# Optimization experiments

Measured on AMD Instinct MI355X. Metric: run time of the kernel, lower is better.

## Reference

```python
import jax, jax.numpy as jnp
import numpy as np

B, T = 4, 1024
L, D_IN = 3, 1024          # num HM-LSTM layers, per-layer hidden size
D = L * D_IN               # concatenated hidden size (3072)
EMB = 2048                 # shared embedding size
N_LIN = 2                  # linear_sizes = [2048, 2048]
OUT = 32000                # vocab
SCALE = 0.02


def setup_inputs() -> dict:
    key = jax.random.key(0)
    ks = jax.random.split(key, 8)
    return {
        "x": jax.random.normal(ks[0], (B, T, D), jnp.float32),
        "w": jax.random.normal(ks[1], (L, D), jnp.float32) * SCALE,        # gate weights, one [D] vector per layer
        "emb_w": jax.random.normal(ks[2], (L, D_IN, EMB), jnp.float32) * SCALE,
        "emb_b": jax.random.normal(ks[3], (L, EMB), jnp.float32) * SCALE,
        "lin_w": jax.random.normal(ks[4], (N_LIN, EMB, EMB), jnp.float32) * SCALE,
        "lin_b": jax.random.normal(ks[5], (N_LIN, EMB), jnp.float32) * SCALE,
        "out_w": jax.random.normal(ks[6], (EMB, OUT), jnp.float32) * SCALE,
        "out_b": jax.random.normal(ks[7], (OUT,), jnp.float32) * SCALE,
    }


def reference(x, w, emb_w, emb_b, lin_w, lin_b, out_w, out_b):
    Bx, Tx, Dx = x.shape
    # Per-layer scalar gates: sg_l = h @ w_l, g = sigmoid(sg)  -> [B, T, L]
    g = jax.nn.sigmoid(jnp.einsum('btd,ld->btl', x, w))
    # Split concatenated hidden into layers: [B, T, L, D_IN]
    xl = x.reshape(Bx, Tx, L, D_IN)
    # s = sum_l Linear_l(h_l * g_l); biases sum across layers
    s = jnp.einsum('btl,btli,lie->bte', g, xl, emb_w) + emb_b.sum(axis=0)
    h = jax.nn.relu(s)
    # fnn: stacked linears with tanh activation after each
    for i in range(lin_w.shape[0]):
        h = jnp.tanh(h @ lin_w[i] + lin_b[i])
    # final output projection
    return h @ out_w + out_b
```

## Files before the change

kernel.cpp:

```cpp
#include <hip/hip_runtime.h>
#include <math.h>

typedef __attribute__((ext_vector_type(8))) short short8;
typedef __attribute__((ext_vector_type(8))) unsigned short ushort8;
typedef __attribute__((ext_vector_type(4))) unsigned short ushort4v;
typedef __attribute__((ext_vector_type(4))) unsigned int uint4v;
typedef __attribute__((ext_vector_type(4))) float f32x4;
typedef __attribute__((ext_vector_type(16))) float f32x16;

__device__ __forceinline__ unsigned short f2bf(float f) {
  union { float f; unsigned u; } v; v.f = f;
  unsigned u = v.u;
  return (unsigned short)((u + 0x7fffu + ((u >> 16) & 1u)) >> 16);
}

__device__ __forceinline__ void gload_lds16(const void* g, void* lds) {
  __builtin_amdgcn_global_load_lds(
      (const __attribute__((address_space(1))) unsigned int*)g,
      (__attribute__((address_space(3))) unsigned int*)lds, 16, 0, 0);
}

__device__ __forceinline__ void tc_body(const float* __restrict__ in,
                                        unsigned short* __restrict__ outp,
                                        int R, int C, int r0, int c0,
                                        char* smem) {
  float (*tile)[65] = (float(*)[65])smem;
  const int t = threadIdx.x;
  const int tr = t >> 4;
  const int tc = (t & 15) * 4;
#pragma unroll
  for (int p = 0; p < 4; ++p) {
    int r = p * 16 + tr;
    f32x4 v = *(const f32x4*)(in + (size_t)(r0 + r) * C + c0 + tc);
    tile[r][tc] = v[0]; tile[r][tc + 1] = v[1];
    tile[r][tc + 2] = v[2]; tile[r][tc + 3] = v[3];
  }
  __syncthreads();
  const int c = t >> 2;
  const int rb = (t & 3) * 16;
  ushort8 o0, o1;
#pragma unroll
  for (int j = 0; j < 8; ++j) o0[j] = f2bf(tile[rb + j][c]);
#pragma unroll
  for (int j = 0; j < 8; ++j) o1[j] = f2bf(tile[rb + 8 + j][c]);
  unsigned short* dst = outp + (size_t)(c0 + c) * R + r0 + rb;
  *(ushort8*)dst = o0;
  *(ushort8*)(dst + 8) = o1;
}

__global__ __launch_bounds__(256)
void gates_or_tc(const float* __restrict__ x, const float* __restrict__ w,
                 unsigned short* __restrict__ xg,
                 const float* __restrict__ emb_w, unsigned short* __restrict__ emb_wT,
                 const float* __restrict__ lin_w,
                 unsigned short* __restrict__ lin_wT0,
                 unsigned short* __restrict__ lin_wT1) {
  __shared__ __align__(16) char smem[64 * 65 * 4];
  __shared__ float sred[4][3];
  const int bid = blockIdx.x;
  const int t = threadIdx.x;

  if (bid >= 4096) {
    int b2 = bid - 4096;
    if (b2 < 1536) {
      tc_body(emb_w, emb_wT, 3072, 2048, (b2 >> 5) * 64, (b2 & 31) * 64, smem);
    } else {
      int b3 = b2 - 1536;
      const float* in = (b3 < 1024) ? lin_w : (lin_w + 2048 * 2048);
      unsigned short* outp = (b3 < 1024) ? lin_wT0 : lin_wT1;
      b3 &= 1023;
      tc_body(in, outp, 2048, 2048, (b3 >> 5) * 64, (b3 & 31) * 64, smem);
    }
    return;
  }

  const int n = bid;
  const float* xr = x + (size_t)n * 3072;
  f32x4 xv[3];
#pragma unroll
  for (int c = 0; c < 3; ++c)
    xv[c] = *(const f32x4*)(xr + c * 1024 + t * 4);

  float p[3] = {0.f, 0.f, 0.f};
#pragma unroll
  for (int l = 0; l < 3; ++l) {
#pragma unroll
    for (int c = 0; c < 3; ++c) {
      f32x4 wv = *(const f32x4*)(w + l * 3072 + c * 1024 + t * 4);
      p[l] += xv[c][0] * wv[0] + xv[c][1] * wv[1] + xv[c][2] * wv[2] + xv[c][3] * wv[3];
    }
  }
#pragma unroll
  for (int off = 32; off; off >>= 1) {
    p[0] += __shfl_xor(p[0], off);
    p[1] += __shfl_xor(p[1], off);
    p[2] += __shfl_xor(p[2], off);
  }
  const int wave = t >> 6, lane = t & 63;
  if (lane == 0) {
    sred[wave][0] = p[0]; sred[wave][1] = p[1]; sred[wave][2] = p[2];
  }
  __syncthreads();
  float g[3];
#pragma unroll
  for (int l = 0; l < 3; ++l) {
    float s = sred[0][l] + sred[1][l] + sred[2][l] + sred[3][l];
    g[l] = 1.f / (1.f + expf(-s));
  }
  unsigned short* orow = xg + (size_t)n * 3072;
#pragma unroll
  for (int c = 0; c < 3; ++c) {
    ushort4v o;
#pragma unroll
    for (int j = 0; j < 4; ++j) o[j] = f2bf(xv[c][j] * g[c]);
    *(ushort4v*)(orow + c * 1024 + t * 4) = o;
  }
}

__global__ __launch_bounds__(256)
void gemm0_or_tc(const unsigned short* __restrict__ A,
                 const unsigned short* __restrict__ Bt,
                 const float* __restrict__ bias,
                 unsigned short* __restrict__ Cb,
                 const float* __restrict__ tc_in,
                 unsigned short* __restrict__ tc_out,
                 int do_tc) {
  __shared__ __align__(16) char smem[32768];
  const int bid = blockIdx.x;

  if (bid >= 512) {
    int b2 = bid - 512;
    tc_body(tc_in, tc_out, 2048, 32000, (b2 / 500) * 64, (b2 % 500) * 64, smem);
    return;
  }
  (void)do_tc;

  unsigned short* As = (unsigned short*)smem;
  unsigned short* Bs = (unsigned short*)(smem + 16384);
  constexpr int K = 3072, N = 2048;

  const int tid = threadIdx.x;
  const int lane = tid & 63;
  const int wv = tid >> 6;
  const int wm = wv >> 1, wn = wv & 1;
  const int lid = (bid & 7) * 64 + (bid >> 3);
  const int mt = lid & 31;
  const int nt = lid >> 5;
  const int m0 = mt * 128, n0 = nt * 128;
  const size_t strideB = (size_t)K * 2;

  f32x4 acc[4][4] = {};

  for (int kt = 0; kt < K; kt += 64) {
    __syncthreads();
#pragma unroll
    for (int i = 0; i < 4; ++i) {
      const int o = wv * 4096 + i * 1024 + lane * 16;
      const int row = o >> 7;
      const int sw = (((o >> 4) & 7) * 16) ^ ((row & 7) << 4);
      gload_lds16((const char*)A + (size_t)(m0 + row) * strideB + (size_t)kt * 2 + sw,
                  (char*)As + wv * 4096 + i * 1024);
      gload_lds16((const char*)Bt + (size_t)(n0 + row) * strideB + (size_t)kt * 2 + sw,
                  (char*)Bs + wv * 4096 + i * 1024);
    }
    __syncthreads();
#pragma unroll
    for (int kk = 0; kk < 2; ++kk) {
      short8 av[4], bv[4];
      const int kb = kk * 64 + (lane >> 4) * 16;
#pragma unroll
      for (int mi = 0; mi < 4; ++mi) {
        int row = wm * 64 + mi * 16 + (lane & 15);
        av[mi] = *(const short8*)((const char*)As + row * 128 + (kb ^ ((row & 7) << 4)));
      }
#pragma unroll
      for (int ni = 0; ni < 4; ++ni) {
        int row = wn * 64 + ni * 16 + (lane & 15);
        bv[ni] = *(const short8*)((const char*)Bs + row * 128 + (kb ^ ((row & 7) << 4)));
      }
#pragma unroll
      for (int mi = 0; mi < 4; ++mi)
#pragma unroll
        for (int ni = 0; ni < 4; ++ni)
          acc[mi][ni] = __builtin_amdgcn_mfma_f32_16x16x32_bf16(av[mi], bv[ni], acc[mi][ni], 0, 0, 0);
    }
  }

  const int lr = lane >> 4, lc = lane & 15;
#pragma unroll
  for (int ni = 0; ni < 4; ++ni) {
    int c = n0 + wn * 64 + ni * 16 + lc;
    float bb = bias[c] + bias[N + c] + bias[2 * N + c];
#pragma unroll
    for (int mi = 0; mi < 4; ++mi) {
      int r0 = m0 + wm * 64 + mi * 16 + lr * 4;
      f32x4 v = acc[mi][ni];
#pragma unroll
      for (int j = 0; j < 4; ++j) {
        float val = v[j] + bb;
        val = val > 0.f ? val : 0.f;
        Cb[(size_t)(r0 + j) * N + c] = f2bf(val);
      }
    }
  }
}

template <int EPI>
__global__ __launch_bounds__(256)
void gemm_tt(const unsigned short* __restrict__ A,
             const unsigned short* __restrict__ Bt,
             const float* __restrict__ bias,
             unsigned short* __restrict__ Cb,
             float* __restrict__ Cf,
             int K, int N) {
  __shared__ __align__(16) unsigned short As[128 * 64];
  __shared__ __align__(16) unsigned short Bs[128 * 64];

  const int tid = threadIdx.x;
  const int lane = tid & 63;
  const int wv = tid >> 6;
  const int wm = wv >> 1, wn = wv & 1;
  const int bid = blockIdx.x;
  const int cpx = gridDim.x >> 3;
  const int lid = (bid & 7) * cpx + (bid >> 3);
  const int mt = lid & 31;
  const int nt = lid >> 5;
  const int m0 = mt * 128, n0 = nt * 128;
  const size_t strideB = (size_t)K * 2;

  f32x4 acc[4][4] = {};

  for (int kt = 0; kt < K; kt += 64) {
    __syncthreads();
#pragma unroll
    for (int i = 0; i < 4; ++i) {
      const int o = wv * 4096 + i * 1024 + lane * 16;
      const int row = o >> 7;
      const int sw = (((o >> 4) & 7) * 16) ^ ((row & 7) << 4);
      gload_lds16((const char*)A + (size_t)(m0 + row) * strideB + (size_t)kt * 2 + sw,
                  (char*)As + wv * 4096 + i * 1024);
      gload_lds16((const char*)Bt + (size_t)(n0 + row) * strideB + (size_t)kt * 2 + sw,
                  (char*)Bs + wv * 4096 + i * 1024);
    }
    __syncthreads();
#pragma unroll
    for (int kk = 0; kk < 2; ++kk) {
      short8 av[4], bv[4];
      const int kb = kk * 64 + (lane >> 4) * 16;
#pragma unroll
      for (int mi = 0; mi < 4; ++mi) {
        int row = wm * 64 + mi * 16 + (lane & 15);
        av[mi] = *(const short8*)((const char*)As + row * 128 + (kb ^ ((row & 7) << 4)));
      }
#pragma unroll
      for (int ni = 0; ni < 4; ++ni) {
        int row = wn * 64 + ni * 16 + (lane & 15);
        bv[ni] = *(const short8*)((const char*)Bs + row * 128 + (kb ^ ((row & 7) << 4)));
      }
#pragma unroll
      for (int mi = 0; mi < 4; ++mi)
#pragma unroll
        for (int ni = 0; ni < 4; ++ni)
          acc[mi][ni] = __builtin_amdgcn_mfma_f32_16x16x32_bf16(av[mi], bv[ni], acc[mi][ni], 0, 0, 0);
    }
  }

  const int lr = lane >> 4, lc = lane & 15;
#pragma unroll
  for (int ni = 0; ni < 4; ++ni) {
    int c = n0 + wn * 64 + ni * 16 + lc;
    float bb;
    if (EPI == 0) bb = bias[c] + bias[N + c] + bias[2 * N + c];
    else          bb = bias[c];
#pragma unroll
    for (int mi = 0; mi < 4; ++mi) {
      int r0 = m0 + wm * 64 + mi * 16 + lr * 4;
      f32x4 v = acc[mi][ni];
#pragma unroll
      for (int j = 0; j < 4; ++j) {
        float val = v[j] + bb;
        size_t idx = (size_t)(r0 + j) * N + c;
        if (EPI == 0) { val = val > 0.f ? val : 0.f; Cb[idx] = f2bf(val); }
        else if (EPI == 1) { Cb[idx] = f2bf(tanhf(val)); }
        else { Cf[idx] = val; }
      }
    }
  }
}

__global__ __launch_bounds__(512, 2)
void gemm8_out(const unsigned short* __restrict__ A,
               const unsigned short* __restrict__ Bt,
               const float* __restrict__ bias,
               float* __restrict__ Cf,
               int K, int N) {
  __shared__ __align__(16) unsigned short As8[2][256 * 64];
  __shared__ __align__(16) unsigned short Bs8[2][256 * 64];

  const int tid = threadIdx.x;
  const int lane = tid & 63;
  const int wid = tid >> 6;
  const int wm = wid >> 2, wn = wid & 3;

  const int bid = blockIdx.x;
  const int cpx = gridDim.x >> 3;
  const int lid = (bid & 7) * cpx + (bid >> 3);
  const int mt = lid & 15;
  const int ntile = lid >> 4;
  const int m0 = mt * 256, n0 = ntile * 256;
  const size_t strideB = (size_t)K * 2;
  const int kTiles = K >> 6;

  const unsigned short* smat = (wid < 4) ? A : Bt;
  char* sb = (wid < 4) ? (char*)As8 : (char*)Bs8;
  const int part = wid & 3;
  const int srow0 = ((wid < 4) ? m0 : n0) + part * 64 + (lane >> 3);
  const int ssw = ((lane & 7) ^ (lane >> 3)) << 4;

  auto stage8 = [&](int buf, int t) {
#pragma unroll
    for (int i = 0; i < 8; ++i)
      gload_lds16((const char*)smat + (size_t)(srow0 + i * 8) * strideB +
                      (size_t)t * 128 + ssw,
                  sb + buf * 32768 + part * 8192 + i * 1024);
  };

  const int l31 = lane & 31;
  const int hk16 = (lane >> 5) * 16;

  f32x16 acc[4][2] = {};

  stage8(0, 0);
  stage8(1, 1);
  asm volatile("s_waitcnt vmcnt(8)" ::: "memory");
  __builtin_amdgcn_sched_barrier(0);
  __builtin_amdgcn_s_barrier();

  for (int t = 0; t < kTiles; ++t) {
    const char* ab = (const char*)As8 + (t & 1) * 32768;
    const char* bb = (const char*)Bs8 + (t & 1) * 32768;
    short8 av[2][4], bva[4], bvb[4];

#pragma unroll
    for (int mi = 0; mi < 2; ++mi) {
      int r = wm * 128 + mi * 32 + l31;
      int sz = (r & 7) << 4;
#pragma unroll
      for (int ks = 0; ks < 4; ++ks)
        av[mi][ks] = *(const short8*)(ab + r * 128 + ((ks * 32 + hk16) ^ sz));
    }
    {
      int r = wn * 64 + l31;
      int sz = (r & 7) << 4;
#pragma unroll
      for (int ks = 0; ks < 4; ++ks)
        bva[ks] = *(const short8*)(bb + r * 128 + ((ks * 32 + hk16) ^ sz));
    }
    __builtin_amdgcn_s_setprio(1);
#pragma unroll
    for (int ks = 0; ks < 4; ++ks)
#pragma unroll
      for (int mi = 0; mi < 2; ++mi)
        acc[mi][0] = __builtin_amdgcn_mfma_f32_32x32x16_bf16(
            av[mi][ks], bva[ks], acc[mi][0], 0, 0, 0);
    __builtin_amdgcn_s_setprio(0);

    {
      int r = wn * 64 + 32 + l31;
      int sz = (r & 7) << 4;
#pragma unroll
      for (int ks = 0; ks < 4; ++ks)
        bvb[ks] = *(const short8*)(bb + r * 128 + ((ks * 32 + hk16) ^ sz));
    }
    __builtin_amdgcn_s_setprio(1);
#pragma unroll
    for (int ks = 0; ks < 4; ++ks)
#pragma unroll
      for (int mi = 0; mi < 2; ++mi)
        acc[mi][1] = __builtin_amdgcn_mfma_f32_32x32x16_bf16(
            av[mi][ks], bvb[ks], acc[mi][1], 0, 0, 0);
    __builtin_amdgcn_s_setprio(0);

#pragma unroll
    for (int mi = 0; mi < 2; ++mi) {
      int r = wm * 128 + 64 + mi * 32 + l31;
      int sz = (r & 7) << 4;
#pragma unroll
      for (int ks = 0; ks < 4; ++ks)
        av[mi][ks] = *(const short8*)(ab + r * 128 + ((ks * 32 + hk16) ^ sz));
    }
    __builtin_amdgcn_s_setprio(1);
#pragma unroll
    for (int ks = 0; ks < 4; ++ks)
#pragma unroll
      for (int mi = 0; mi < 2; ++mi)
        acc[2 + mi][1] = __builtin_amdgcn_mfma_f32_32x32x16_bf16(
            av[mi][ks], bvb[ks], acc[2 + mi][1], 0, 0, 0);
    __builtin_amdgcn_s_setprio(0);

    __builtin_amdgcn_s_setprio(1);
#pragma unroll
    for (int ks = 0; ks < 4; ++ks)
#pragma unroll
      for (int mi = 0; mi < 2; ++mi)
        acc[2 + mi][0] = __builtin_amdgcn_mfma_f32_32x32x16_bf16(
            av[mi][ks], bva[ks], acc[2 + mi][0], 0, 0, 0);
    __builtin_amdgcn_s_setprio(0);

    if (t + 1 < kTiles) {
      __builtin_amdgcn_sched_barrier(0);
      __builtin_amdgcn_s_barrier();
      if (t + 2 < kTiles) {
        stage8(t & 1, t + 2);
        asm volatile("s_waitcnt vmcnt(8)" ::: "memory");
      } else {
        asm volatile("s_waitcnt vmcnt(0)" ::: "memory");
      }
      __builtin_amdgcn_sched_barrier(0);
      __builtin_amdgcn_s_barrier();
    }
  }

  const int rbase = m0 + wm * 128 + 4 * (lane >> 5);
#pragma unroll
  for (int ni = 0; ni < 2; ++ni) {
    int c = n0 + wn * 64 + ni * 32 + l31;
    float bb2 = bias[c];
#pragma unroll
    for (int mi = 0; mi < 4; ++mi) {
#pragma unroll
      for (int rg = 0; rg < 16; ++rg) {
        int r = rbase + mi * 32 + (rg & 3) + 8 * (rg >> 2);
        __builtin_nontemporal_store(acc[mi][ni][rg] + bb2,
                                    &Cf[(size_t)r * N + c]);
      }
    }
  }
}

template <int EPI>
__global__ __launch_bounds__(256)
void gemm_bf16(const unsigned short* __restrict__ A,
               const float* __restrict__ B,
               const float* __restrict__ bias,
               unsigned short* __restrict__ Cb,
               float* __restrict__ Cf,
               int K, int N) {
  __shared__ __align__(16) unsigned short As[128 * 64];
  __shared__ __align__(16) unsigned short Bs[128 * 64];

  const int tid = threadIdx.x;
  const int lane = tid & 63;
  const int wv = tid >> 6;
  const int wm = wv >> 1, wn = wv & 1;
  const int mt = blockIdx.x & 31;
  const int nt = blockIdx.x >> 5;
  const int m0 = mt * 128, n0 = nt * 128;

  f32x4 acc[4][4] = {};

  for (int kt = 0; kt < K; kt += 64) {
    __syncthreads();
#pragma unroll
    for (int i = 0; i < 4; ++i) {
      int q = tid + 256 * i;
      int row = q >> 3;
      int kc = q & 7;
      uint4v v = *(const uint4v*)((const char*)A +
                   ((size_t)(m0 + row) * K + kt) * 2 + kc * 16);
      *(uint4v*)((char*)As + row * 128 + ((kc * 16) ^ ((row & 7) << 4))) = v;
    }
#pragma unroll
    for (int gi = 0; gi < 4; ++gi) {
      int q = tid + 256 * gi;
      int nn = q & 127;
      int k8 = q >> 7;
      const float* src = B + (size_t)(kt + k8 * 8) * N + (n0 + nn);
      ushort8 tv;
#pragma unroll
      for (int j = 0; j < 8; ++j) tv[j] = f2bf(src[(size_t)j * N]);
      *(ushort8*)((char*)Bs + nn * 128 + ((k8 * 16) ^ ((nn & 7) << 4))) = tv;
    }
    __syncthreads();
#pragma unroll
    for (int kk = 0; kk < 2; ++kk) {
      short8 av[4], bv[4];
      const int kb = kk * 64 + (lane >> 4) * 16;
#pragma unroll
      for (int mi = 0; mi < 4; ++mi) {
        int row = wm * 64 + mi * 16 + (lane & 15);
        av[mi] = *(const short8*)((const char*)As + row * 128 + (kb ^ ((row & 7) << 4)));
      }
#pragma unroll
      for (int ni = 0; ni < 4; ++ni) {
        int row = wn * 64 + ni * 16 + (lane & 15);
        bv[ni] = *(const short8*)((const char*)Bs + row * 128 + (kb ^ ((row & 7) << 4)));
      }
#pragma unroll
      for (int mi = 0; mi < 4; ++mi)
#pragma unroll
        for (int ni = 0; ni < 4; ++ni)
          acc[mi][ni] = __builtin_amdgcn_mfma_f32_16x16x32_bf16(av[mi], bv[ni], acc[mi][ni], 0, 0, 0);
    }
  }

  const int lr = lane >> 4, lc = lane & 15;
#pragma unroll
  for (int ni = 0; ni < 4; ++ni) {
    int c = n0 + wn * 64 + ni * 16 + lc;
    float bb = bias[c];
#pragma unroll
    for (int mi = 0; mi < 4; ++mi) {
      int r0 = m0 + wm * 64 + mi * 16 + lr * 4;
      f32x4 v = acc[mi][ni];
#pragma unroll
      for (int j = 0; j < 4; ++j) {
        float val = v[j] + bb;
        size_t idx = (size_t)(r0 + j) * N + c;
        if (EPI == 1) { Cb[idx] = f2bf(tanhf(val)); }
        else { Cf[idx] = val; }
      }
    }
  }
}

extern "C" void kernel_launch(void* const* d_in, const int* in_sizes, int n_in,
                              void* d_out, int out_size, void* d_ws, size_t ws_size,
                              hipStream_t stream) {
  const float* x     = (const float*)d_in[0];
  const float* w     = (const float*)d_in[1];
  const float* emb_w = (const float*)d_in[2];
  const float* emb_b = (const float*)d_in[3];
  const float* lin_w = (const float*)d_in[4];
  const float* lin_b = (const float*)d_in[5];
  const float* out_w = (const float*)d_in[6];
  const float* out_b = (const float*)d_in[7];
  float* out = (float*)d_out;

  char* ob = (char*)d_out;
  unsigned short* xg      = (unsigned short*)ob;
  unsigned short* h0      = (unsigned short*)(ob + (((size_t)128) << 20));
  unsigned short* h1      = (unsigned short*)(ob + (((size_t)160) << 20));
  unsigned short* emb_wT  = (unsigned short*)(ob + (((size_t)192) << 20));
  unsigned short* lin_wT0 = (unsigned short*)(ob + (((size_t)208) << 20));
  unsigned short* lin_wT1 = (unsigned short*)(ob + (((size_t)224) << 20));
  unsigned short* h2      = (unsigned short*)d_ws;
  unsigned short* out_wT  = (unsigned short*)((char*)d_ws + (((size_t)32) << 20));
  const bool fast4 = ws_size >= ((((size_t)32) << 20) + (size_t)32000 * 2048 * 2);

  gates_or_tc<<<4096 + 3584, 256, 0, stream>>>(x, w, xg, emb_w, emb_wT,
                                               lin_w, lin_wT0, lin_wT1);
  if (fast4)
    gemm0_or_tc<<<512 + 16000, 256, 0, stream>>>(xg, emb_wT, emb_b, h0,
                                                 out_w, out_wT, 1);
  else
    gemm0_or_tc<<<512, 256, 0, stream>>>(xg, emb_wT, emb_b, h0,
                                         out_w, out_wT, 0);

  gemm_tt<1><<<32 * 16, 256, 0, stream>>>(h0, lin_wT0, lin_b, h1, nullptr, 2048, 2048);
  gemm_tt<1><<<32 * 16, 256, 0, stream>>>(h1, lin_wT1, lin_b + 2048, h2, nullptr, 2048, 2048);
  if (fast4)
    gemm8_out<<<16 * 125, 512, 0, stream>>>(h2, out_wT, out_b, out, 2048, 32000);
  else
    gemm_bf16<2><<<32 * 250, 256, 0, stream>>>(h2, out_w, out_b, nullptr, out, 2048, 32000);
}
```

Before: 885.6 us.

## Shrink output GEMM tile to 256x128 with K-step 32 for higher occupancy

Reworks the final vocab projection kernel from 256x256 tiles with K-step 64 to 256x128 tiles with K-step 32. Each wave now owns a 64x64 sub-tile, loading is spread across all 8 waves with a new swizzle, and LDS usage drops so up to four blocks can reside per CU. The grid doubles to 4000 blocks. The aim is better occupancy and latency hiding, at the cost of lower arithmetic intensity per block, more barriers per unit of K, and re-reading the A matrix twice as often.

```diff
diff --git a/kernel.cpp b/kernel.cpp
--- a/kernel.cpp
+++ b/kernel.cpp
@@ -288,131 +288,96 @@
   }
 }
 
-__global__ __launch_bounds__(512, 2)
+__global__ __launch_bounds__(512, 4)
 void gemm8_out(const unsigned short* __restrict__ A,
                const unsigned short* __restrict__ Bt,
                const float* __restrict__ bias,
                float* __restrict__ Cf,
                int K, int N) {
-  __shared__ __align__(16) unsigned short As8[2][256 * 64];
-  __shared__ __align__(16) unsigned short Bs8[2][256 * 64];
+  __shared__ __align__(16) unsigned short As8[2][256 * 32];
+  __shared__ __align__(16) unsigned short Bs8[2][128 * 32];
 
   const int tid = threadIdx.x;
   const int lane = tid & 63;
   const int wid = tid >> 6;
-  const int wm = wid >> 2, wn = wid & 3;
+  const int wm = wid >> 1, wn = wid & 1;
 
   const int bid = blockIdx.x;
   const int cpx = gridDim.x >> 3;
   const int lid = (bid & 7) * cpx + (bid >> 3);
   const int mt = lid & 15;
   const int ntile = lid >> 4;
-  const int m0 = mt * 256, n0 = ntile * 256;
+  const int m0 = mt * 256, n0 = ntile * 128;
   const size_t strideB = (size_t)K * 2;
-  const int kTiles = K >> 6;
-
-  const unsigned short* smat = (wid < 4) ? A : Bt;
-  char* sb = (wid < 4) ? (char*)As8 : (char*)Bs8;
-  const int part = wid & 3;
-  const int srow0 = ((wid < 4) ? m0 : n0) + part * 64 + (lane >> 3);
-  const int ssw = ((lane & 7) ^ (lane >> 3)) << 4;
-
-  auto stage8 = [&](int buf, int t) {
-#pragma unroll
-    for (int i = 0; i < 8; ++i)
-      gload_lds16((const char*)smat + (size_t)(srow0 + i * 8) * strideB +
-                      (size_t)t * 128 + ssw,
-                  sb + buf * 32768 + part * 8192 + i * 1024);
+  const int kTiles = K >> 5;
+
+  const int srow = lane >> 2;
+  const int schunk = (lane & 3) ^ (srow & 3);
+
+  auto stage = [&](int buf, int t) {
+#pragma unroll
+    for (int j = 0; j < 3; ++j) {
+      const int q = wid * 3 + j;
+      if (q < 16)
+        gload_lds16((const char*)A + (size_t)(m0 + q * 16 + srow) * strideB +
+                        (size_t)t * 64 + schunk * 16,
+                    (char*)As8 + buf * 16384 + q * 1024);
+      else
+        gload_lds16((const char*)Bt + (size_t)(n0 + (q - 16) * 16 + srow) * strideB +
+                        (size_t)t * 64 + schunk * 16,
+                    (char*)Bs8 + buf * 8192 + (q - 16) * 1024);
+    }
   };
 
   const int l31 = lane & 31;
   const int hk16 = (lane >> 5) * 16;
 
-  f32x16 acc[4][2] = {};
-
-  stage8(0, 0);
-  stage8(1, 1);
-  asm volatile("s_waitcnt vmcnt(8)" ::: "memory");
+  f32x16 acc[2][2] = {};
+
+  stage(0, 0);
+  stage(1, 1);
+  asm volatile("s_waitcnt vmcnt(3)" ::: "memory");
   __builtin_amdgcn_sched_barrier(0);
   __builtin_amdgcn_s_barrier();
 
   for (int t = 0; t < kTiles; ++t) {
-    const char* ab = (const char*)As8 + (t & 1) * 32768;
-    const char* bb = (const char*)Bs8 + (t & 1) * 32768;
-    short8 av[2][4], bva[4], bvb[4];
+    const char* ab = (const char*)As8 + (t & 1) * 16384;
+    const char* bb = (const char*)Bs8 + (t & 1) * 8192;
+    short8 av[2][2], bv[2][2];
 
 #pragma unroll
     for (int mi = 0; mi < 2; ++mi) {
-      int r = wm * 128 + mi * 32 + l31;
-      int sz = (r & 7) << 4;
-#pragma unroll
-      for (int ks = 0; ks < 4; ++ks)
-        av[mi][ks] = *(const short8*)(ab + r * 128 + ((ks * 32 + hk16) ^ sz));
-    }
-    {
-      int r = wn * 64 + l31;
-      int sz = (r & 7) << 4;
-#pragma unroll
-      for (int ks = 0; ks < 4; ++ks)
-        bva[ks] = *(const short8*)(bb + r * 128 + ((ks * 32 + hk16) ^ sz));
+      int r = wm * 64 + mi * 32 + l31;
+      int sz = (r & 3) << 4;
+#pragma unroll
+      for (int ks = 0; ks < 2; ++ks)
+        av[mi][ks] = *(const short8*)(ab + r * 64 + ((ks * 32 + hk16) ^ sz));
+    }
+#pragma unroll
+    for (int ni = 0; ni < 2; ++ni) {
+      int r = wn * 64 + ni * 32 + l31;
+      int sz = (r & 3) << 4;
+#pragma unroll
+      for (int ks = 0; ks < 2; ++ks)
+        bv[ni][ks] = *(const short8*)(bb + r * 64 + ((ks * 32 + hk16) ^ sz));
     }
     __builtin_amdgcn_s_setprio(1);
 #pragma unroll
-    for (int ks = 0; ks < 4; ++ks)
+    for (int ks = 0; ks < 2; ++ks)
 #pragma unroll
       for (int mi = 0; mi < 2; ++mi)
-        acc[mi][0] = __builtin_amdgcn_mfma_f32_32x32x16_bf16(
-            av[mi][ks], bva[ks], acc[mi][0], 0, 0, 0);
-    __builtin_amdgcn_s_setprio(0);
-
-    {
-      int r = wn * 64 + 32 + l31;
-      int sz = (r & 7) << 4;
-#pragma unroll
-      for (int ks = 0; ks < 4; ++ks)
-        bvb[ks] = *(const short8*)(bb + r * 128 + ((ks * 32 + hk16) ^ sz));
-    }
-    __builtin_amdgcn_s_setprio(1);
-#pragma unroll
-    for (int ks = 0; ks < 4; ++ks)
-#pragma unroll
-      for (int mi = 0; mi < 2; ++mi)
-        acc[mi][1] = __builtin_amdgcn_mfma_f32_32x32x16_bf16(
-            av[mi][ks], bvb[ks], acc[mi][1], 0, 0, 0);
-    __builtin_amdgcn_s_setprio(0);
-
-#pragma unroll
-    for (int mi = 0; mi < 2; ++mi) {
-      int r = wm * 128 + 64 + mi * 32 + l31;
-      int sz = (r & 7) << 4;
-#pragma unroll
-      for (int ks = 0; ks < 4; ++ks)
-        av[mi][ks] = *(const short8*)(ab + r * 128 + ((ks * 32 + hk16) ^ sz));
-    }
-    __builtin_amdgcn_s_setprio(1);
-#pragma unroll
-    for (int ks = 0; ks < 4; ++ks)
-#pragma unroll
-      for (int mi = 0; mi < 2; ++mi)
-        acc[2 + mi][1] = __builtin_amdgcn_mfma_f32_32x32x16_bf16(
-            av[mi][ks], bvb[ks], acc[2 + mi][1], 0, 0, 0);
-    __builtin_amdgcn_s_setprio(0);
-
-    __builtin_amdgcn_s_setprio(1);
-#pragma unroll
-    for (int ks = 0; ks < 4; ++ks)
-#pragma unroll
-      for (int mi = 0; mi < 2; ++mi)
-        acc[2 + mi][0] = __builtin_amdgcn_mfma_f32_32x32x16_bf16(
-            av[mi][ks], bva[ks], acc[2 + mi][0], 0, 0, 0);
+#pragma unroll
+        for (int ni = 0; ni < 2; ++ni)
+          acc[mi][ni] = __builtin_amdgcn_mfma_f32_32x32x16_bf16(
+              av[mi][ks], bv[ni][ks], acc[mi][ni], 0, 0, 0);
     __builtin_amdgcn_s_setprio(0);
 
     if (t + 1 < kTiles) {
       __builtin_amdgcn_sched_barrier(0);
       __builtin_amdgcn_s_barrier();
       if (t + 2 < kTiles) {
-        stage8(t & 1, t + 2);
-        asm volatile("s_waitcnt vmcnt(8)" ::: "memory");
+        stage(t & 1, t + 2);
+        asm volatile("s_waitcnt vmcnt(3)" ::: "memory");
       } else {
         asm volatile("s_waitcnt vmcnt(0)" ::: "memory");
       }
@@ -421,13 +386,13 @@
     }
   }
 
-  const int rbase = m0 + wm * 128 + 4 * (lane >> 5);
+  const int rbase = m0 + wm * 64 + 4 * (lane >> 5);
 #pragma unroll
   for (int ni = 0; ni < 2; ++ni) {
     int c = n0 + wn * 64 + ni * 32 + l31;
     float bb2 = bias[c];
 #pragma unroll
-    for (int mi = 0; mi < 4; ++mi) {
+    for (int mi = 0; mi < 2; ++mi) {
 #pragma unroll
       for (int rg = 0; rg < 16; ++rg) {
         int r = rbase + mi * 32 + (rg & 3) + 8 * (rg >> 2);
@@ -560,7 +525,7 @@
   gemm_tt<1><<<32 * 16, 256, 0, stream>>>(h0, lin_wT0, lin_b, h1, nullptr, 2048, 2048);
   gemm_tt<1><<<32 * 16, 256, 0, stream>>>(h1, lin_wT1, lin_b + 2048, h2, nullptr, 2048, 2048);
   if (fast4)
-    gemm8_out<<<16 * 125, 512, 0, stream>>>(h2, out_wT, out_b, out, 2048, 32000);
+    gemm8_out<<<16 * 250, 512, 0, stream>>>(h2, out_wT, out_b, out, 2048, 32000);
   else
     gemm_bf16<2><<<32 * 250, 256, 0, stream>>>(h2, out_w, out_b, nullptr, out, 2048, 32000);
 }
```

Result: slower. 987.9 us (+11.6%).
